# Performance work log

Hardware: AMD Instinct MI355X
Metric: run time of the kernel (lower is better)

The kernel has to match this reference:

```python
import jax, jax.numpy as jnp
import numpy as np

N, C, H, W = 8, 32, 48, 48
S, K, OC = 2, 3, 32  # scale_int, kernel_size, out_channels
HID = 256
FEAT = C * K * K  # 288


def setup_inputs() -> dict:
    key = jax.random.key(0)
    ks = jax.random.split(key, 5)
    F_LR = jax.random.normal(ks[0], (N, C, H, W), dtype=jnp.float32)
    v = jax.random.normal(ks[1], (H * S * W * S, 3), dtype=jnp.float32)
    w1 = jax.random.normal(ks[2], (3, HID), dtype=jnp.float32) * 0.2
    b1 = jnp.zeros((HID,), dtype=jnp.float32)
    w2 = jax.random.normal(ks[3], (HID, FEAT * OC), dtype=jnp.float32) * 0.02
    b2 = jnp.zeros((FEAT * OC,), dtype=jnp.float32)
    return {"F_LR": F_LR, "v": v, "w1": w1, "b1": b1, "w2": w2, "b2": b2}


def _unfold(x, k):
    # torch F.unfold(x, k, padding=1): (N, C*k*k, H*W), channel-major then (ki,kj)
    n, c, h, w = x.shape
    xp = jnp.pad(x, ((0, 0), (0, 0), (1, 1), (1, 1)))
    cols = [xp[:, :, i:i + h, j:j + w] for i in range(k) for j in range(k)]
    p = jnp.stack(cols, axis=2)  # (N, C, k*k, H, W)
    return p.reshape(n, c * k * k, h * w)


def reference(F_LR, v, w1, b1, w2, b2):
    n = F_LR.shape[0]
    # weight prediction MLP
    hmid = jax.nn.relu(v @ w1 + b1)
    W_pred = hmid @ w2 + b2  # (H*S*W*S, C*K*K*OC)
    # reshape like torch: view(H,S,W,S,FEAT,OC).permute(1,3,0,2,4,5) -> (S*S, H*W, FEAT, OC)
    Wt = (W_pred.reshape(H, S, W, S, FEAT, OC)
          .transpose(1, 3, 0, 2, 4, 5)
          .reshape(S * S, H * W, FEAT, OC))
    # add_dimensions replicates F_LR S*S times, so patches are shared across p
    pat = _unfold(F_LR, K)  # (N, FEAT, H*W)
    # per-pixel tiny matmul: out[n,p,l,o] = sum_f pat[n,f,l] * Wt[p,l,f,o]
    out = jnp.einsum('nfl,plfo->nplo', pat, Wt)  # (N, S*S, H*W, OC)
    # assemble upsampled image: p=(sh,sw), pixel (h*S+sh, w*S+sw)
    out = (out.reshape(n, S, S, H, W, OC)
           .transpose(0, 5, 3, 1, 4, 2)
           .reshape(n, OC, S * H, S * W))
    # integer scale => create_mask is all-True, masked_select is identity
    return out
```

## Files before the change

### kernel.cpp

```cpp
#include <hip/hip_runtime.h>
#include <hip/hip_bf16.h>

#define NN    8
#define CC    32
#define HH    48
#define WW    48
#define OCC   32
#define HID   256
#define FEAT  288
#define RTOT  9216
#define COLS  9216
#define XUP   96
#define YUP   96
#define OUTSZ (NN*OCC*XUP*YUP)

using bf16x8 = __attribute__((ext_vector_type(8))) __bf16;
using bf16x4 = __attribute__((ext_vector_type(4))) __bf16;
using f32x4  = __attribute__((ext_vector_type(4))) float;

#define GLOAD_LDS16(gp, lp)                                                        \
  __builtin_amdgcn_global_load_lds((const __attribute__((address_space(1))) void*)(gp), \
                                   (__attribute__((address_space(3))) void*)(lp), 16, 0, 0)

__global__ void prep_hmid(const float* __restrict__ v, const float* __restrict__ w1,
                          const float* __restrict__ b1, __hip_bfloat16* __restrict__ hmidp) {
  int r = blockIdx.x;
  int t = threadIdx.x;
  float v0 = v[r*3+0], v1 = v[r*3+1], v2 = v[r*3+2];
  float val = v0*w1[t] + v1*w1[HID+t] + v2*w1[2*HID+t] + b1[t];
  val = fmaxf(val, 0.0f);
  int dst = ((r>>4)*8 + (t>>5))*512 + ((t>>3)&3)*128 + (r&15)*8 + (t&7);
  hmidp[dst] = __float2bfloat16(val);
}

__global__ void prep_w2(const float* __restrict__ w2, __hip_bfloat16* __restrict__ w2p) {
  int idx = blockIdx.x*256 + threadIdx.x;
  int k   = idx / COLS;
  int col = idx % COLS;
  float val = w2[idx];
  int colchunk = col >> 7;
  int cg   = (col >> 4) & 7;
  int lane = (((k>>3)&3)<<4) | (col & 15);
  int kb   = k >> 5;
  int i    = k & 7;
  int dst  = (((colchunk*8 + kb)*8 + cg)*64 + lane)*8 + i;
  w2p[dst] = __float2bfloat16(val);
}

#define BARRIER_LGKM() do {                              \
    asm volatile("s_waitcnt lgkmcnt(0)" ::: "memory");   \
    __builtin_amdgcn_sched_barrier(0);                   \
    __builtin_amdgcn_s_barrier();                        \
  } while (0)

#define ISSUE_HALF(SET, CH, H) do {                                              \
    const char* _b = w2base + ((size_t)((CH)*8 + (H)*4))*8192 + wv*2048          \
                     + (size_t)lane*16;                                          \
    _Pragma("unroll")                                                            \
    for (int _i = 0; _i < 4; ++_i) {                                             \
      SET[0][_i] = *(const bf16x8*)(_b + _i*8192);                               \
      SET[1][_i] = *(const bf16x8*)(_b + _i*8192 + 1024);                        \
    }                                                                            \
  } while (0)

__launch_bounds__(256, 2)
__global__ void fused_main(const float* __restrict__ F_LR,
                           const __hip_bfloat16* __restrict__ hmidp,
                           const __hip_bfloat16* __restrict__ w2p,
                           const float* __restrict__ b2,
                           float* __restrict__ outp,
                           int G, int nch) {
  extern __shared__ __align__(16) char smem[];
  char*   AtileB = smem;
  __bf16* patB   = (__bf16*)(smem + 16384);
  float*  wc     = (float*)(smem + 44032);
  __bf16* biasL  = (__bf16*)(smem + 60416);

  const int tid  = threadIdx.x;
  const int lane = tid & 63;
  const int wv   = tid >> 6;
  const int blk  = blockIdx.x;
  int rowtile, g;
  if (G == 2) {
    int xcd = blk & 7;
    int j   = blk >> 3;
    g       = xcd & 1;
    rowtile = (xcd >> 1)*72 + j;
  } else {
    rowtile = blk;
    g       = 0;
  }
  const int X  = rowtile / 3;
  const int Yh = rowtile - X*3;
  const int h  = X >> 1;
  const int w0 = Yh * 16;
  const int l15 = lane & 15;
  const int qt  = lane >> 4;
  const int oc  = lane & 31;
  const int nh  = lane >> 5;

  const char* w2base = (const char*)w2p + (size_t)g*nch*65536;

  {
    const char* hsrc = (const char*)hmidp + (size_t)rowtile*16384;
    #pragma unroll
    for (int j = 0; j < 4; ++j)
      GLOAD_LDS16(hsrc + j*4096 + wv*1024 + lane*16, AtileB + j*4096 + wv*1024);
  }

  for (int i = tid; i < nch*128; i += 256)
    biasL[i] = (__bf16)b2[g*nch*128 + i];

  {
    const int n = tid >> 5, c = tid & 31;
    const float* fsrc = F_LR + ((size_t)(n*CC + c)*HH)*WW;
    #pragma unroll
    for (int ki = 0; ki < 3; ++ki) {
      int hh = h - 1 + ki;
      bool hok = (unsigned)hh < (unsigned)HH;
      #pragma unroll
      for (int wi = 0; wi < 18; ++wi) {
        int ww = w0 - 1 + wi;
        float val = (hok && (unsigned)ww < (unsigned)WW) ? fsrc[hh*WW + ww] : 0.f;
        patB[((c*3 + ki)*18 + wi)*8 + n] = (__bf16)val;
      }
    }
  }
  asm volatile("s_waitcnt vmcnt(0) lgkmcnt(0)" ::: "memory");
  __builtin_amdgcn_sched_barrier(0);
  __builtin_amdgcn_s_barrier();

  float oacc[8][4];
  #pragma unroll
  for (int i = 0; i < 8; ++i)
    { oacc[i][0]=0.f; oacc[i][1]=0.f; oacc[i][2]=0.f; oacc[i][3]=0.f; }

  bf16x8 bA[2][4], bB[2][4];
  ISSUE_HALF(bA, 0, 0);
  ISSUE_HALF(bB, 0, 1);

  for (int ch = 0; ch < nch; ++ch) {
    f32x4 acc00 = {0,0,0,0}, acc01 = {0,0,0,0}, acc10 = {0,0,0,0}, acc11 = {0,0,0,0};

    #pragma unroll
    for (int s = 0; s < 4; ++s) {
      bf16x8 a0 = *(const bf16x8*)(AtileB + s*1024 + lane*16);
      bf16x8 a1 = *(const bf16x8*)(AtileB + 8192 + s*1024 + lane*16);
      acc00 = __builtin_amdgcn_mfma_f32_16x16x32_bf16(a0, bA[0][s], acc00, 0,0,0);
      acc01 = __builtin_amdgcn_mfma_f32_16x16x32_bf16(a0, bA[1][s], acc01, 0,0,0);
      acc10 = __builtin_amdgcn_mfma_f32_16x16x32_bf16(a1, bA[0][s], acc10, 0,0,0);
      acc11 = __builtin_amdgcn_mfma_f32_16x16x32_bf16(a1, bA[1][s], acc11, 0,0,0);
    }
    if (ch + 1 < nch) { ISSUE_HALF(bA, ch+1, 0); }

    #pragma unroll
    for (int s = 0; s < 4; ++s) {
      bf16x8 a0 = *(const bf16x8*)(AtileB + (4+s)*1024 + lane*16);
      bf16x8 a1 = *(const bf16x8*)(AtileB + 8192 + (4+s)*1024 + lane*16);
      acc00 = __builtin_amdgcn_mfma_f32_16x16x32_bf16(a0, bB[0][s], acc00, 0,0,0);
      acc01 = __builtin_amdgcn_mfma_f32_16x16x32_bf16(a0, bB[1][s], acc01, 0,0,0);
      acc10 = __builtin_amdgcn_mfma_f32_16x16x32_bf16(a1, bB[0][s], acc10, 0,0,0);
      acc11 = __builtin_amdgcn_mfma_f32_16x16x32_bf16(a1, bB[1][s], acc11, 0,0,0);
    }
    if (ch + 1 < nch) { ISSUE_HALF(bB, ch+1, 1); }

    {
      float bias0 = (float)biasL[ch*128 + wv*32 + l15];
      float bias1 = (float)biasL[ch*128 + wv*32 + 16 + l15];
      #pragma unroll
      for (int mg = 0; mg < 2; ++mg) {
        #pragma unroll
        for (int ng = 0; ng < 2; ++ng) {
          f32x4 A = (mg==0) ? (ng==0?acc00:acc01) : (ng==0?acc10:acc11);
          float bb = ng ? bias1 : bias0;
          A[0]+=bb; A[1]+=bb; A[2]+=bb; A[3]+=bb;
          int ocx  = ng*16 + l15;
          int ridx = (mg*16 + qt*4) ^ ((ocx&7)<<2);
          *(f32x4*)&wc[wv*1024 + ocx*32 + ridx] = A;
        }
      }
    }
    BARRIER_LGKM();

    const int swz = (oc & 7) << 2;
    #pragma unroll
    for (int fl = 0; fl < 4; ++fl) {
      const int f   = (g*nch + ch)*4 + fl;
      const int c   = f / 9;
      const int rem = f - c*9;
      const int ki  = rem / 3;
      const int kj  = rem - ki*3;
      const f32x4 wlo = *(const f32x4*)&wc[fl*1024 + oc*32 + ((wv*8    ) ^ swz)];
      const f32x4 whi = *(const f32x4*)&wc[fl*1024 + oc*32 + ((wv*8 + 4) ^ swz)];
      const __bf16* pbase = patB + (c*3 + ki)*18*8 + nh*4;
      #pragma unroll
      for (int rrh = 0; rrh < 4; ++rrh) {
        bf16x4 pq = *(const bf16x4*)(pbase + (wv*4 + rrh + kj)*8);
        float w0v = (rrh < 2) ? ((rrh == 0) ? wlo[0] : wlo[2]) : ((rrh == 2) ? whi[0] : whi[2]);
        float w1v = (rrh < 2) ? ((rrh == 0) ? wlo[1] : wlo[3]) : ((rrh == 2) ? whi[1] : whi[3]);
        #pragma unroll
        for (int q = 0; q < 4; ++q) {
          float pv = (float)pq[q];
          oacc[rrh*2][q]   += w0v * pv;
          oacc[rrh*2+1][q] += w1v * pv;
        }
      }
    }
    BARRIER_LGKM();
  }

  float* OP = outp + (size_t)g*OUTSZ;
  #pragma unroll
  for (int q = 0; q < 4; ++q) {
    int n = nh*4 + q;
    f32x4 v0, v1;
    v0[0]=oacc[0][q]; v0[1]=oacc[1][q]; v0[2]=oacc[2][q]; v0[3]=oacc[3][q];
    v1[0]=oacc[4][q]; v1[1]=oacc[5][q]; v1[2]=oacc[6][q]; v1[3]=oacc[7][q];
    float* dst = OP + (((size_t)(n*OCC + oc)*XUP + X)*YUP + Yh*32 + wv*8);
    *(f32x4*)dst     = v0;
    *(f32x4*)(dst+4) = v1;
  }
}

__global__ void reduce2(const float* __restrict__ P, float* __restrict__ out) {
  int i = blockIdx.x*256 + threadIdx.x;
  if (i < OUTSZ/4) {
    f32x4 a = ((const f32x4*)P)[i];
    f32x4 b = ((const f32x4*)(P + OUTSZ))[i];
    ((f32x4*)out)[i] = a + b;
  }
}

extern "C" void kernel_launch(void* const* d_in, const int* in_sizes, int n_in,
                              void* d_out, int out_size, void* d_ws, size_t ws_size,
                              hipStream_t stream) {
  const float* F_LR = (const float*)d_in[0];
  const float* v    = (const float*)d_in[1];
  const float* w1   = (const float*)d_in[2];
  const float* b1   = (const float*)d_in[3];
  const float* w2   = (const float*)d_in[4];
  const float* b2   = (const float*)d_in[5];
  float* out = (float*)d_out;

  const size_t prepBytes = (size_t)RTOT*HID*2;
  const size_t need2 = 2*prepBytes + 2ull*OUTSZ*4;
  const int G   = (ws_size >= need2) ? 2 : 1;
  const int nch = 72 / G;

  __hip_bfloat16* hmidp = (__hip_bfloat16*)d_ws;
  __hip_bfloat16* w2p   = (__hip_bfloat16*)((char*)d_ws + prepBytes);
  float* P = (float*)((char*)d_ws + 2*prepBytes);
  float* target = (G == 2) ? P : out;

  const size_t shmem = 16384 + 27648 + 16384 + (size_t)nch*128*2;

  hipLaunchKernelGGL(prep_hmid, dim3(RTOT), dim3(HID), 0, stream, v, w1, b1, hmidp);
  hipLaunchKernelGGL(prep_w2,   dim3((HID*COLS)/256), dim3(256), 0, stream, w2, w2p);
  hipLaunchKernelGGL(fused_main, dim3(288*G), dim3(256), shmem, stream,
                     F_LR, hmidp, w2p, b2, target, G, nch);
  if (G == 2)
    hipLaunchKernelGGL(reduce2, dim3(OUTSZ/4/256), dim3(256), 0, stream, P, out);
}
```

Before: 174.7 us.

## Keep MFMA results in registers and contract patches per wave, reducing once at end

Each wave now owns one feature f per chunk and applies the patch contraction directly on its MFMA accumulator registers. This removes the per-chunk LDS staging of predicted weights and the two block barriers per chunk. Partial sums from the four waves are combined once through LDS at the end. The register double-buffered prefetch of w2 is replaced by direct loads inside the k loop, and bias is read from global memory. The trade-off is a larger register accumulator (64 floats per lane), which can reduce occupancy, and less overlap of the w2 loads.

```diff
diff --git a/kernel.cpp b/kernel.cpp
--- a/kernel.cpp
+++ b/kernel.cpp
@@ -15,8 +15,8 @@
 #define OUTSZ (NN*OCC*XUP*YUP)
 
 using bf16x8 = __attribute__((ext_vector_type(8))) __bf16;
-using bf16x4 = __attribute__((ext_vector_type(4))) __bf16;
 using f32x4  = __attribute__((ext_vector_type(4))) float;
+using f32x2  = __attribute__((ext_vector_type(2))) float;
 
 #define GLOAD_LDS16(gp, lp)                                                        \
   __builtin_amdgcn_global_load_lds((const __attribute__((address_space(1))) void*)(gp), \
@@ -47,22 +47,6 @@
   w2p[dst] = __float2bfloat16(val);
 }
 
-#define BARRIER_LGKM() do {                              \
-    asm volatile("s_waitcnt lgkmcnt(0)" ::: "memory");   \
-    __builtin_amdgcn_sched_barrier(0);                   \
-    __builtin_amdgcn_s_barrier();                        \
-  } while (0)
-
-#define ISSUE_HALF(SET, CH, H) do {                                              \
-    const char* _b = w2base + ((size_t)((CH)*8 + (H)*4))*8192 + wv*2048          \
-                     + (size_t)lane*16;                                          \
-    _Pragma("unroll")                                                            \
-    for (int _i = 0; _i < 4; ++_i) {                                             \
-      SET[0][_i] = *(const bf16x8*)(_b + _i*8192);                               \
-      SET[1][_i] = *(const bf16x8*)(_b + _i*8192 + 1024);                        \
-    }                                                                            \
-  } while (0)
-
 __launch_bounds__(256, 2)
 __global__ void fused_main(const float* __restrict__ F_LR,
                            const __hip_bfloat16* __restrict__ hmidp,
@@ -73,8 +57,6 @@
   extern __shared__ __align__(16) char smem[];
   char*   AtileB = smem;
   __bf16* patB   = (__bf16*)(smem + 16384);
-  float*  wc     = (float*)(smem + 44032);
-  __bf16* biasL  = (__bf16*)(smem + 60416);
 
   const int tid  = threadIdx.x;
   const int lane = tid & 63;
@@ -96,8 +78,6 @@
   const int w0 = Yh * 16;
   const int l15 = lane & 15;
   const int qt  = lane >> 4;
-  const int oc  = lane & 31;
-  const int nh  = lane >> 5;
 
   const char* w2base = (const char*)w2p + (size_t)g*nch*65536;
 
@@ -107,9 +87,6 @@
     for (int j = 0; j < 4; ++j)
       GLOAD_LDS16(hsrc + j*4096 + wv*1024 + lane*16, AtileB + j*4096 + wv*1024);
   }
-
-  for (int i = tid; i < nch*128; i += 256)
-    biasL[i] = (__bf16)b2[g*nch*128 + i];
 
   {
     const int n = tid >> 5, c = tid & 31;
@@ -126,99 +103,102 @@
       }
     }
   }
-  asm volatile("s_waitcnt vmcnt(0) lgkmcnt(0)" ::: "memory");
-  __builtin_amdgcn_sched_barrier(0);
-  __builtin_amdgcn_s_barrier();
-
-  float oacc[8][4];
+  __syncthreads();
+
+  f32x2 oacc2[8][2][4];
   #pragma unroll
-  for (int i = 0; i < 8; ++i)
-    { oacc[i][0]=0.f; oacc[i][1]=0.f; oacc[i][2]=0.f; oacc[i][3]=0.f; }
-
-  bf16x8 bA[2][4], bB[2][4];
-  ISSUE_HALF(bA, 0, 0);
-  ISSUE_HALF(bB, 0, 1);
+  for (int n = 0; n < 8; ++n)
+    #pragma unroll
+    for (int mg = 0; mg < 2; ++mg)
+      #pragma unroll
+      for (int j = 0; j < 4; ++j) oacc2[n][mg][j] = 0.f;
 
   for (int ch = 0; ch < nch; ++ch) {
+    const int f   = (g*nch + ch)*4 + wv;
+    const int c   = f / 9;
+    const int rem = f - c*9;
+    const int ki  = rem / 3;
+    const int kj  = rem - ki*3;
+    const float bias0 = b2[f*32 + l15];
+    const float bias1 = b2[f*32 + 16 + l15];
+
     f32x4 acc00 = {0,0,0,0}, acc01 = {0,0,0,0}, acc10 = {0,0,0,0}, acc11 = {0,0,0,0};
-
-    #pragma unroll
-    for (int s = 0; s < 4; ++s) {
-      bf16x8 a0 = *(const bf16x8*)(AtileB + s*1024 + lane*16);
-      bf16x8 a1 = *(const bf16x8*)(AtileB + 8192 + s*1024 + lane*16);
-      acc00 = __builtin_amdgcn_mfma_f32_16x16x32_bf16(a0, bA[0][s], acc00, 0,0,0);
-      acc01 = __builtin_amdgcn_mfma_f32_16x16x32_bf16(a0, bA[1][s], acc01, 0,0,0);
-      acc10 = __builtin_amdgcn_mfma_f32_16x16x32_bf16(a1, bA[0][s], acc10, 0,0,0);
-      acc11 = __builtin_amdgcn_mfma_f32_16x16x32_bf16(a1, bA[1][s], acc11, 0,0,0);
-    }
-    if (ch + 1 < nch) { ISSUE_HALF(bA, ch+1, 0); }
-
-    #pragma unroll
-    for (int s = 0; s < 4; ++s) {
-      bf16x8 a0 = *(const bf16x8*)(AtileB + (4+s)*1024 + lane*16);
-      bf16x8 a1 = *(const bf16x8*)(AtileB + 8192 + (4+s)*1024 + lane*16);
-      acc00 = __builtin_amdgcn_mfma_f32_16x16x32_bf16(a0, bB[0][s], acc00, 0,0,0);
-      acc01 = __builtin_amdgcn_mfma_f32_16x16x32_bf16(a0, bB[1][s], acc01, 0,0,0);
-      acc10 = __builtin_amdgcn_mfma_f32_16x16x32_bf16(a1, bB[0][s], acc10, 0,0,0);
-      acc11 = __builtin_amdgcn_mfma_f32_16x16x32_bf16(a1, bB[1][s], acc11, 0,0,0);
-    }
-    if (ch + 1 < nch) { ISSUE_HALF(bB, ch+1, 1); }
-
-    {
-      float bias0 = (float)biasL[ch*128 + wv*32 + l15];
-      float bias1 = (float)biasL[ch*128 + wv*32 + 16 + l15];
-      #pragma unroll
-      for (int mg = 0; mg < 2; ++mg) {
+    #pragma unroll
+    for (int kb = 0; kb < 8; ++kb) {
+      const char* bp = w2base + (size_t)(ch*8 + kb)*8192 + wv*2048 + (size_t)lane*16;
+      bf16x8 b0 = *(const bf16x8*)(bp);
+      bf16x8 b1 = *(const bf16x8*)(bp + 1024);
+      bf16x8 a0 = *(const bf16x8*)(AtileB + kb*1024 + lane*16);
+      bf16x8 a1 = *(const bf16x8*)(AtileB + 8192 + kb*1024 + lane*16);
+      acc00 = __builtin_amdgcn_mfma_f32_16x16x32_bf16(a0, b0, acc00, 0,0,0);
+      acc01 = __builtin_amdgcn_mfma_f32_16x16x32_bf16(a0, b1, acc01, 0,0,0);
+      acc10 = __builtin_amdgcn_mfma_f32_16x16x32_bf16(a1, b0, acc10, 0,0,0);
+      acc11 = __builtin_amdgcn_mfma_f32_16x16x32_bf16(a1, b1, acc11, 0,0,0);
+    }
+
+    const __bf16* prow = patB + (size_t)((c*3 + ki)*18)*8;
+    const int w0i = 2*qt + kj;
+    bf16x8 pw00 = *(const bf16x8*)(prow + (w0i    )*8);
+    bf16x8 pw01 = *(const bf16x8*)(prow + (w0i + 1)*8);
+    bf16x8 pw10 = *(const bf16x8*)(prow + (w0i + 8)*8);
+    bf16x8 pw11 = *(const bf16x8*)(prow + (w0i + 9)*8);
+
+    f32x2 accb[2][4];
+    #pragma unroll
+    for (int j = 0; j < 4; ++j) {
+      accb[0][j][0] = acc00[j] + bias0;  accb[0][j][1] = acc01[j] + bias1;
+      accb[1][j][0] = acc10[j] + bias0;  accb[1][j][1] = acc11[j] + bias1;
+    }
+
+    #pragma unroll
+    for (int n = 0; n < 8; ++n) {
+      float pv00 = (float)pw00[n];
+      float pv01 = (float)pw01[n];
+      float pv10 = (float)pw10[n];
+      float pv11 = (float)pw11[n];
+      oacc2[n][0][0] += accb[0][0] * pv00;
+      oacc2[n][0][1] += accb[0][1] * pv00;
+      oacc2[n][0][2] += accb[0][2] * pv01;
+      oacc2[n][0][3] += accb[0][3] * pv01;
+      oacc2[n][1][0] += accb[1][0] * pv10;
+      oacc2[n][1][1] += accb[1][1] * pv10;
+      oacc2[n][1][2] += accb[1][2] * pv11;
+      oacc2[n][1][3] += accb[1][3] * pv11;
+    }
+  }
+
+  float* redL = (float*)smem;
+  float* OP = outp + (size_t)g*OUTSZ;
+  #pragma unroll
+  for (int np = 0; np < 2; ++np) {
+    #pragma unroll
+    for (int mg = 0; mg < 2; ++mg) {
+      __syncthreads();
+      #pragma unroll
+      for (int q = 0; q < 4; ++q) {
         #pragma unroll
-        for (int ng = 0; ng < 2; ++ng) {
-          f32x4 A = (mg==0) ? (ng==0?acc00:acc01) : (ng==0?acc10:acc11);
-          float bb = ng ? bias1 : bias0;
-          A[0]+=bb; A[1]+=bb; A[2]+=bb; A[3]+=bb;
-          int ocx  = ng*16 + l15;
-          int ridx = (mg*16 + qt*4) ^ ((ocx&7)<<2);
-          *(f32x4*)&wc[wv*1024 + ocx*32 + ridx] = A;
+        for (int comp = 0; comp < 2; ++comp) {
+          f32x4 vv;
+          vv[0] = oacc2[np*4+q][mg][0][comp];
+          vv[1] = oacc2[np*4+q][mg][1][comp];
+          vv[2] = oacc2[np*4+q][mg][2][comp];
+          vv[3] = oacc2[np*4+q][mg][3][comp];
+          *(f32x4*)&redL[(((wv*4 + q)*2 + comp)*64 + lane)*4] = vv;
         }
       }
-    }
-    BARRIER_LGKM();
-
-    const int swz = (oc & 7) << 2;
-    #pragma unroll
-    for (int fl = 0; fl < 4; ++fl) {
-      const int f   = (g*nch + ch)*4 + fl;
-      const int c   = f / 9;
-      const int rem = f - c*9;
-      const int ki  = rem / 3;
-      const int kj  = rem - ki*3;
-      const f32x4 wlo = *(const f32x4*)&wc[fl*1024 + oc*32 + ((wv*8    ) ^ swz)];
-      const f32x4 whi = *(const f32x4*)&wc[fl*1024 + oc*32 + ((wv*8 + 4) ^ swz)];
-      const __bf16* pbase = patB + (c*3 + ki)*18*8 + nh*4;
-      #pragma unroll
-      for (int rrh = 0; rrh < 4; ++rrh) {
-        bf16x4 pq = *(const bf16x4*)(pbase + (wv*4 + rrh + kj)*8);
-        float w0v = (rrh < 2) ? ((rrh == 0) ? wlo[0] : wlo[2]) : ((rrh == 2) ? whi[0] : whi[2]);
-        float w1v = (rrh < 2) ? ((rrh == 0) ? wlo[1] : wlo[3]) : ((rrh == 2) ? whi[1] : whi[3]);
+      __syncthreads();
+      const int n = np*4 + wv;
+      #pragma unroll
+      for (int comp = 0; comp < 2; ++comp) {
+        f32x4 s = *(const f32x4*)&redL[(((0*4 + wv)*2 + comp)*64 + lane)*4];
         #pragma unroll
-        for (int q = 0; q < 4; ++q) {
-          float pv = (float)pq[q];
-          oacc[rrh*2][q]   += w0v * pv;
-          oacc[rrh*2+1][q] += w1v * pv;
-        }
+        for (int w = 1; w < 4; ++w)
+          s += *(const f32x4*)&redL[(((w*4 + wv)*2 + comp)*64 + lane)*4];
+        const int ocx = comp*16 + l15;
+        float* dst = OP + (((size_t)(n*OCC + ocx)*XUP + X)*YUP + Yh*32 + mg*16 + qt*4);
+        *(f32x4*)dst = s;
       }
     }
-    BARRIER_LGKM();
-  }
-
-  float* OP = outp + (size_t)g*OUTSZ;
-  #pragma unroll
-  for (int q = 0; q < 4; ++q) {
-    int n = nh*4 + q;
-    f32x4 v0, v1;
-    v0[0]=oacc[0][q]; v0[1]=oacc[1][q]; v0[2]=oacc[2][q]; v0[3]=oacc[3][q];
-    v1[0]=oacc[4][q]; v1[1]=oacc[5][q]; v1[2]=oacc[6][q]; v1[3]=oacc[7][q];
-    float* dst = OP + (((size_t)(n*OCC + oc)*XUP + X)*YUP + Yh*32 + wv*8);
-    *(f32x4*)dst     = v0;
-    *(f32x4*)(dst+4) = v1;
   }
 }
 
@@ -252,7 +232,7 @@
   float* P = (float*)((char*)d_ws + 2*prepBytes);
   float* target = (G == 2) ? P : out;
 
-  const size_t shmem = 16384 + 27648 + 16384 + (size_t)nch*128*2;
+  const size_t shmem = 16384 + 27648;
 
   hipLaunchKernelGGL(prep_hmid, dim3(RTOT), dim3(HID), 0, stream, v, w1, b1, hmidp);
   hipLaunchKernelGGL(prep_w2,   dim3((HID*COLS)/256), dim3(256), 0, stream, w2, w2p);
```

Result: slower. 270.5 us (+54.8%).

## Merge two output rows per block to share patch and bias loads

Applied to the files above, without the earlier changes.

Each block now has 512 threads and covers two upsampled rows (X=2m and 2m+1) that share the same low-res row h. Two groups of four waves each take their own A tile of hmid. The F_LR patch tile and the bias are loaded once for both rows, and the grid is halved. The aim is to cut redundant patch gathering and bias staging. In exchange, LDS use roughly doubles, which may limit how many blocks fit per CU. Each wave still loads its own w2 fragments, so the w2 bandwidth per output row is unchanged.

```diff
diff --git a/kernel.cpp b/kernel.cpp
--- a/kernel.cpp
+++ b/kernel.cpp
@@ -54,7 +54,7 @@
   } while (0)
 
 #define ISSUE_HALF(SET, CH, H) do {                                              \
-    const char* _b = w2base + ((size_t)((CH)*8 + (H)*4))*8192 + wv*2048          \
+    const char* _b = w2base + ((size_t)((CH)*8 + (H)*4))*8192 + colq*2048        \
                      + (size_t)lane*16;                                          \
     _Pragma("unroll")                                                            \
     for (int _i = 0; _i < 4; ++_i) {                                             \
@@ -63,7 +63,7 @@
     }                                                                            \
   } while (0)
 
-__launch_bounds__(256, 2)
+__launch_bounds__(512, 2)
 __global__ void fused_main(const float* __restrict__ F_LR,
                            const __hip_bfloat16* __restrict__ hmidp,
                            const __hip_bfloat16* __restrict__ w2p,
@@ -72,28 +72,30 @@
                            int G, int nch) {
   extern __shared__ __align__(16) char smem[];
   char*   AtileB = smem;
-  __bf16* patB   = (__bf16*)(smem + 16384);
-  float*  wc     = (float*)(smem + 44032);
-  __bf16* biasL  = (__bf16*)(smem + 60416);
+  __bf16* patB   = (__bf16*)(smem + 32768);
+  float*  wc     = (float*)(smem + 60416);
+  __bf16* biasL  = (__bf16*)(smem + 93184);
 
   const int tid  = threadIdx.x;
   const int lane = tid & 63;
   const int wv   = tid >> 6;
+  const int rg   = wv >> 2;
+  const int colq = wv & 3;
   const int blk  = blockIdx.x;
-  int rowtile, g;
+  int pq, g;
   if (G == 2) {
     int xcd = blk & 7;
     int j   = blk >> 3;
     g       = xcd & 1;
-    rowtile = (xcd >> 1)*72 + j;
+    pq      = (xcd >> 1)*36 + j;
   } else {
-    rowtile = blk;
-    g       = 0;
-  }
-  const int X  = rowtile / 3;
-  const int Yh = rowtile - X*3;
-  const int h  = X >> 1;
-  const int w0 = Yh * 16;
+    pq = blk;
+    g  = 0;
+  }
+  const int m   = pq / 3;
+  const int Yh  = pq - m*3;
+  const int h   = m;
+  const int w0  = Yh * 16;
   const int l15 = lane & 15;
   const int qt  = lane >> 4;
   const int oc  = lane & 31;
@@ -102,29 +104,32 @@
   const char* w2base = (const char*)w2p + (size_t)g*nch*65536;
 
   {
-    const char* hsrc = (const char*)hmidp + (size_t)rowtile*16384;
+    const int t0 = 6*m + Yh;
+    const int tt = (wv < 4) ? t0 : (t0 + 3);
+    const int wq4 = wv & 3;
+    const char* hsrc = (const char*)hmidp + (size_t)tt*16384;
+    char* adst = AtileB + (size_t)(wv >> 2)*16384;
     #pragma unroll
     for (int j = 0; j < 4; ++j)
-      GLOAD_LDS16(hsrc + j*4096 + wv*1024 + lane*16, AtileB + j*4096 + wv*1024);
-  }
-
-  for (int i = tid; i < nch*128; i += 256)
+      GLOAD_LDS16(hsrc + j*4096 + wq4*1024 + lane*16, adst + j*4096 + wq4*1024);
+  }
+
+  for (int i = tid; i < nch*128; i += 512)
     biasL[i] = (__bf16)b2[g*nch*128 + i];
 
-  {
-    const int n = tid >> 5, c = tid & 31;
-    const float* fsrc = F_LR + ((size_t)(n*CC + c)*HH)*WW;
-    #pragma unroll
-    for (int ki = 0; ki < 3; ++ki) {
-      int hh = h - 1 + ki;
-      bool hok = (unsigned)hh < (unsigned)HH;
-      #pragma unroll
-      for (int wi = 0; wi < 18; ++wi) {
-        int ww = w0 - 1 + wi;
-        float val = (hok && (unsigned)ww < (unsigned)WW) ? fsrc[hh*WW + ww] : 0.f;
-        patB[((c*3 + ki)*18 + wi)*8 + n] = (__bf16)val;
-      }
-    }
+  for (int idx = tid; idx < 13824; idx += 512) {
+    int wi = idx % 18;
+    int t4 = idx / 18;
+    int n  = t4 & 7;
+    int t3 = t4 >> 3;
+    int ki = t3 % 3;
+    int c  = t3 / 3;
+    int hh = h - 1 + ki;
+    int ww = w0 - 1 + wi;
+    float val = 0.f;
+    if ((unsigned)hh < (unsigned)HH && (unsigned)ww < (unsigned)WW)
+      val = F_LR[((n*CC + c)*HH + hh)*WW + ww];
+    patB[(t3*18 + wi)*8 + n] = (__bf16)val;
   }
   asm volatile("s_waitcnt vmcnt(0) lgkmcnt(0)" ::: "memory");
   __builtin_amdgcn_sched_barrier(0);
@@ -139,13 +144,15 @@
   ISSUE_HALF(bA, 0, 0);
   ISSUE_HALF(bB, 0, 1);
 
+  const char* Abase = AtileB + (size_t)rg*16384;
+
   for (int ch = 0; ch < nch; ++ch) {
     f32x4 acc00 = {0,0,0,0}, acc01 = {0,0,0,0}, acc10 = {0,0,0,0}, acc11 = {0,0,0,0};
 
     #pragma unroll
     for (int s = 0; s < 4; ++s) {
-      bf16x8 a0 = *(const bf16x8*)(AtileB + s*1024 + lane*16);
-      bf16x8 a1 = *(const bf16x8*)(AtileB + 8192 + s*1024 + lane*16);
+      bf16x8 a0 = *(const bf16x8*)(Abase + s*1024 + lane*16);
+      bf16x8 a1 = *(const bf16x8*)(Abase + 8192 + s*1024 + lane*16);
       acc00 = __builtin_amdgcn_mfma_f32_16x16x32_bf16(a0, bA[0][s], acc00, 0,0,0);
       acc01 = __builtin_amdgcn_mfma_f32_16x16x32_bf16(a0, bA[1][s], acc01, 0,0,0);
       acc10 = __builtin_amdgcn_mfma_f32_16x16x32_bf16(a1, bA[0][s], acc10, 0,0,0);
@@ -155,8 +162,8 @@
 
     #pragma unroll
     for (int s = 0; s < 4; ++s) {
-      bf16x8 a0 = *(const bf16x8*)(AtileB + (4+s)*1024 + lane*16);
-      bf16x8 a1 = *(const bf16x8*)(AtileB + 8192 + (4+s)*1024 + lane*16);
+      bf16x8 a0 = *(const bf16x8*)(Abase + (4+s)*1024 + lane*16);
+      bf16x8 a1 = *(const bf16x8*)(Abase + 8192 + (4+s)*1024 + lane*16);
       acc00 = __builtin_amdgcn_mfma_f32_16x16x32_bf16(a0, bB[0][s], acc00, 0,0,0);
       acc01 = __builtin_amdgcn_mfma_f32_16x16x32_bf16(a0, bB[1][s], acc01, 0,0,0);
       acc10 = __builtin_amdgcn_mfma_f32_16x16x32_bf16(a1, bB[0][s], acc10, 0,0,0);
@@ -165,8 +172,9 @@
     if (ch + 1 < nch) { ISSUE_HALF(bB, ch+1, 1); }
 
     {
-      float bias0 = (float)biasL[ch*128 + wv*32 + l15];
-      float bias1 = (float)biasL[ch*128 + wv*32 + 16 + l15];
+      float bias0 = (float)biasL[ch*128 + colq*32 + l15];
+      float bias1 = (float)biasL[ch*128 + colq*32 + 16 + l15];
+      float* wcb = wc + (size_t)(colq*2 + rg)*1024;
       #pragma unroll
       for (int mg = 0; mg < 2; ++mg) {
         #pragma unroll
@@ -176,7 +184,7 @@
           A[0]+=bb; A[1]+=bb; A[2]+=bb; A[3]+=bb;
           int ocx  = ng*16 + l15;
           int ridx = (mg*16 + qt*4) ^ ((ocx&7)<<2);
-          *(f32x4*)&wc[wv*1024 + ocx*32 + ridx] = A;
+          *(f32x4*)&wcb[ocx*32 + ridx] = A;
         }
       }
     }
@@ -190,17 +198,18 @@
       const int rem = f - c*9;
       const int ki  = rem / 3;
       const int kj  = rem - ki*3;
-      const f32x4 wlo = *(const f32x4*)&wc[fl*1024 + oc*32 + ((wv*8    ) ^ swz)];
-      const f32x4 whi = *(const f32x4*)&wc[fl*1024 + oc*32 + ((wv*8 + 4) ^ swz)];
-      const __bf16* pbase = patB + (c*3 + ki)*18*8 + nh*4;
+      const float* wcb = wc + (size_t)(fl*2 + rg)*1024;
+      const f32x4 wlo = *(const f32x4*)&wcb[oc*32 + ((colq*8    ) ^ swz)];
+      const f32x4 whi = *(const f32x4*)&wcb[oc*32 + ((colq*8 + 4) ^ swz)];
+      const __bf16* pbase = patB + (c*3 + ki)*144 + nh*4;
       #pragma unroll
       for (int rrh = 0; rrh < 4; ++rrh) {
-        bf16x4 pq = *(const bf16x4*)(pbase + (wv*4 + rrh + kj)*8);
+        bf16x4 pq2 = *(const bf16x4*)(pbase + (colq*4 + rrh + kj)*8);
         float w0v = (rrh < 2) ? ((rrh == 0) ? wlo[0] : wlo[2]) : ((rrh == 2) ? whi[0] : whi[2]);
         float w1v = (rrh < 2) ? ((rrh == 0) ? wlo[1] : wlo[3]) : ((rrh == 2) ? whi[1] : whi[3]);
         #pragma unroll
         for (int q = 0; q < 4; ++q) {
-          float pv = (float)pq[q];
+          float pv = (float)pq2[q];
           oacc[rrh*2][q]   += w0v * pv;
           oacc[rrh*2+1][q] += w1v * pv;
         }
@@ -210,13 +219,14 @@
   }
 
   float* OP = outp + (size_t)g*OUTSZ;
+  const int X = 2*m + rg;
   #pragma unroll
   for (int q = 0; q < 4; ++q) {
     int n = nh*4 + q;
     f32x4 v0, v1;
     v0[0]=oacc[0][q]; v0[1]=oacc[1][q]; v0[2]=oacc[2][q]; v0[3]=oacc[3][q];
     v1[0]=oacc[4][q]; v1[1]=oacc[5][q]; v1[2]=oacc[6][q]; v1[3]=oacc[7][q];
-    float* dst = OP + (((size_t)(n*OCC + oc)*XUP + X)*YUP + Yh*32 + wv*8);
+    float* dst = OP + (((size_t)(n*OCC + oc)*XUP + X)*YUP + Yh*32 + colq*8);
     *(f32x4*)dst     = v0;
     *(f32x4*)(dst+4) = v1;
   }
@@ -252,11 +262,11 @@
   float* P = (float*)((char*)d_ws + 2*prepBytes);
   float* target = (G == 2) ? P : out;
 
-  const size_t shmem = 16384 + 27648 + 16384 + (size_t)nch*128*2;
+  const size_t shmem = 32768 + 27648 + 32768 + (size_t)nch*128*2;
 
   hipLaunchKernelGGL(prep_hmid, dim3(RTOT), dim3(HID), 0, stream, v, w1, b1, hmidp);
   hipLaunchKernelGGL(prep_w2,   dim3((HID*COLS)/256), dim3(256), 0, stream, w2, w2p);
-  hipLaunchKernelGGL(fused_main, dim3(288*G), dim3(256), shmem, stream,
+  hipLaunchKernelGGL(fused_main, dim3(144*G), dim3(512), shmem, stream,
                      F_LR, hmidp, w2p, b2, target, G, nch);
   if (G == 2)
     hipLaunchKernelGGL(reduce2, dim3(OUTSZ/4/256), dim3(256), 0, stream, P, out);
```

New measurement: 213.0 us. 1.22x slower.
